# Performance work log

Measured on AMD Instinct MI355X. Metric: run time of the kernel, lower is better.

## Reference

```python
import jax, jax.numpy as jnp
import numpy as np

N = 100000        # number of nodes
D_IN = 256        # input feature dim
D_OUT = 128       # output feature dim
NNZ_X = 3200000   # features_nonzero
NNZ_A = 3200000   # adjacency nnz (avg degree 32)
DROPOUT = 0.1


def setup_inputs() -> dict:
    key = jax.random.key(0)
    ks = jax.random.split(key, 7)
    x_rows = jax.random.randint(ks[0], (NNZ_X,), 0, N, dtype=jnp.int32)
    x_cols = jax.random.randint(ks[1], (NNZ_X,), 0, D_IN, dtype=jnp.int32)
    x_vals = jax.random.normal(ks[2], (NNZ_X,), dtype=jnp.float32)
    adj_rows = jax.random.randint(ks[3], (NNZ_A,), 0, N, dtype=jnp.int32)
    adj_cols = jax.random.randint(ks[4], (NNZ_A,), 0, N, dtype=jnp.int32)
    adj_vals = jax.random.uniform(ks[5], (NNZ_A,), dtype=jnp.float32)  # normalized-adj-like positive weights
    W = jax.random.normal(ks[6], (D_IN, D_OUT), dtype=jnp.float32) * 0.05  # 'random_normal' init
    return {"x_rows": x_rows, "x_cols": x_cols, "x_vals": x_vals,
            "adj_rows": adj_rows, "adj_cols": adj_cols, "adj_vals": adj_vals,
            "W": W}


def reference(x_rows, x_cols, x_vals, adj_rows, adj_cols, adj_vals, W):
    keep_prob = 1.0 - DROPOUT
    # tf: dropout_mask = floor(keep_prob + uniform) -> Bernoulli(keep_prob) in {0,1}
    mask = jnp.floor(keep_prob + jax.random.uniform(jax.random.key(42), x_vals.shape, dtype=x_vals.dtype))
    xv = x_vals * mask * (1.0 / keep_prob)  # sparse dropout: retain + rescale
    # SpMM 1: x @ W  -> h [N, D_OUT]; gather W rows by column index, scatter-add by row index
    h = jax.ops.segment_sum(xv[:, None] * W[x_cols], x_rows, num_segments=N)
    # SpMM 2: adj @ h -> out [N, D_OUT]
    out = jax.ops.segment_sum(adj_vals[:, None] * h[adj_cols], adj_rows, num_segments=N)
    return jax.nn.relu(out)
```

## Files before the change

kernel.cpp:

```cpp
#include <hip/hip_runtime.h>
#include <hip/hip_fp16.h>
#include <stdint.h>

constexpr int kN    = 100000;
constexpr int kDOut = 128;
constexpr int kDIn  = 256;
constexpr int kNNZ  = 3200000;
constexpr float kInvKeep = (float)(1.0 / 0.9);
constexpr int kCopies = 8;

typedef __attribute__((ext_vector_type(8))) short short8v;
typedef __attribute__((ext_vector_type(4))) float f32x4;

__device__ __forceinline__ uint32_t rotl32(uint32_t v, int r) {
  return (v << r) | (v >> (32 - r));
}
__device__ __forceinline__ void threefry2x32(uint32_t k0, uint32_t k1,
                                             uint32_t x0, uint32_t x1,
                                             uint32_t& o0, uint32_t& o1) {
  const uint32_t ks0 = k0, ks1 = k1, ks2 = k0 ^ k1 ^ 0x1BD11BDAu;
  x0 += ks0; x1 += ks1;
#define TF_RND(r) { x0 += x1; x1 = rotl32(x1, (r)); x1 ^= x0; }
  TF_RND(13) TF_RND(15) TF_RND(26) TF_RND(6)
  x0 += ks1; x1 += ks2 + 1u;
  TF_RND(17) TF_RND(29) TF_RND(16) TF_RND(24)
  x0 += ks2; x1 += ks0 + 2u;
  TF_RND(13) TF_RND(15) TF_RND(26) TF_RND(6)
  x0 += ks0; x1 += ks1 + 3u;
  TF_RND(17) TF_RND(29) TF_RND(16) TF_RND(24)
  x0 += ks1; x1 += ks2 + 4u;
  TF_RND(13) TF_RND(15) TF_RND(26) TF_RND(6)
  x0 += ks2; x1 += ks0 + 5u;
#undef TF_RND
  o0 = x0; o1 = x1;
}
__device__ __forceinline__ float keep_mask(uint32_t i) {
  uint32_t o0, o1;
  threefry2x32(0u, 42u, 0u, i, o0, o1);
  uint32_t bits = o0 ^ o1;
  float u = __uint_as_float((bits >> 9) | 0x3f800000u) - 1.0f;
  return floorf(0.9f + u);
}

__device__ __forceinline__ uint32_t f32_to_bf16(float f) {
  uint32_t u = __float_as_uint(f);
  u += 0x7fffu + ((u >> 16) & 1u);
  return u >> 16;
}
__device__ __forceinline__ float bf16lo_to_f32(uint32_t packed) {
  return __uint_as_float(packed << 16);
}
__device__ __forceinline__ float bf16hi_to_f32(uint32_t packed) {
  return __uint_as_float(packed & 0xffff0000u);
}

__global__ void wpack_frag_kernel(const float* __restrict__ W,
                                  uint32_t* __restrict__ Wt) {
  int i = blockIdx.x * blockDim.x + threadIdx.x;
  if (i >= kDIn * kDOut / 2) return;
  int jj   = i & 3;
  int lane = (i >> 2) & 63;
  int ks   = (i >> 8) & 7;
  int nt   = i >> 11;
  int n = nt * 16 + (lane & 15);
  int k = ks * 32 + ((lane >> 4) * 8) + 2 * jj;
  uint32_t lo = f32_to_bf16(W[(size_t)k * kDOut + n]);
  uint32_t hi = f32_to_bf16(W[(size_t)(k + 1) * kDOut + n]);
  Wt[i] = lo | (hi << 16);
}

__global__ void scatteradd_kernel(const int* __restrict__ rows,
                                  const int* __restrict__ cols,
                                  const float* __restrict__ vals,
                                  float* __restrict__ Xd, int nnz) {
  int e = blockIdx.x * blockDim.x + threadIdx.x;
  if (e >= nnz) return;
  if (keep_mask((uint32_t)e) == 0.0f) return;
  atomicAdd(&Xd[(size_t)rows[e] * kDIn + cols[e]], vals[e] * kInvKeep);
}

__global__ void __launch_bounds__(256) gemm_mfma_kernel(
    const float* __restrict__ Xd, const uint32_t* __restrict__ Wt,
    uint16_t* __restrict__ hb) {
  const int tid = threadIdx.x;
  const int gw = blockIdx.x * 4 + (tid >> 6);
  if (gw >= kN / 16) return;
  const int lane = tid & 63;
  const int row16 = gw * 16;
  const float* xrow = Xd + (size_t)(row16 + (lane & 15)) * kDIn + ((lane >> 4) * 8);

  f32x4 acc[8];
  #pragma unroll
  for (int nt = 0; nt < 8; ++nt) acc[nt] = f32x4{0.f, 0.f, 0.f, 0.f};

  #pragma unroll
  for (int ks = 0; ks < 8; ++ks) {
    float4 xa = *(const float4*)(xrow + ks * 32);
    float4 xb = *(const float4*)(xrow + ks * 32 + 4);
    short8v a;
    a[0] = (short)f32_to_bf16(xa.x); a[1] = (short)f32_to_bf16(xa.y);
    a[2] = (short)f32_to_bf16(xa.z); a[3] = (short)f32_to_bf16(xa.w);
    a[4] = (short)f32_to_bf16(xb.x); a[5] = (short)f32_to_bf16(xb.y);
    a[6] = (short)f32_to_bf16(xb.z); a[7] = (short)f32_to_bf16(xb.w);
    const uint32_t* bbase = Wt + ks * 256 + lane * 4;
    #pragma unroll
    for (int nt = 0; nt < 8; ++nt) {
      short8v b = *(const short8v*)(bbase + nt * 2048);
      acc[nt] = __builtin_amdgcn_mfma_f32_16x16x32_bf16(a, b, acc[nt], 0, 0, 0);
    }
  }

  const int r0 = row16 + (lane >> 4) * 4;
  const int c0 = lane & 15;
  #pragma unroll
  for (int nt = 0; nt < 8; ++nt) {
    #pragma unroll
    for (int rg = 0; rg < 4; ++rg) {
      hb[(size_t)(r0 + rg) * kDOut + nt * 16 + c0] =
          (uint16_t)f32_to_bf16(acc[nt][rg]);
    }
  }
}

__global__ void hist8_kernel(const int* __restrict__ rows, int* __restrict__ cnt8,
                             int nnz) {
  int e = blockIdx.x * blockDim.x + threadIdx.x;
  if (e >= nnz) return;
  int k = blockIdx.x & (kCopies - 1);
  atomicAdd(&cnt8[k * kN + rows[e]], 1);
}

constexpr int kScanChunk = 2048;
constexpr int kScanBlk   = (kN + kScanChunk - 1) / kScanChunk;

__global__ void scan1_kernel(const int* __restrict__ cnt8, int* __restrict__ rowptr,
                             int* __restrict__ partials, int n) {
  __shared__ int sd[256];
  int b = blockIdx.x, t = threadIdx.x;
  int base = b * kScanChunk + t * 8;
  int v[8]; int s = 0;
  #pragma unroll
  for (int k = 0; k < 8; ++k) {
    int idx = base + k;
    int c = 0;
    if (idx < n) {
      #pragma unroll
      for (int j = 0; j < kCopies; ++j) c += cnt8[j * kN + idx];
    }
    v[k] = c; s += c;
  }
  sd[t] = s; __syncthreads();
  #pragma unroll
  for (int off = 1; off < 256; off <<= 1) {
    int x = (t >= off) ? sd[t - off] : 0;
    __syncthreads();
    sd[t] += x;
    __syncthreads();
  }
  if (t == 255) partials[b] = sd[255];
  int run = (t == 0) ? 0 : sd[t - 1];
  #pragma unroll
  for (int k = 0; k < 8; ++k) { int idx = base + k; if (idx < n) rowptr[idx] = run; run += v[k]; }
}

__global__ void scan2_kernel(int* __restrict__ partials, int* __restrict__ rowptr,
                             int nblk, int n) {
  __shared__ int sd[64];
  int t = threadIdx.x;
  sd[t] = (t < nblk) ? partials[t] : 0;
  __syncthreads();
  #pragma unroll
  for (int off = 1; off < 64; off <<= 1) {
    int x = (t >= off) ? sd[t - off] : 0;
    __syncthreads();
    sd[t] += x;
    __syncthreads();
  }
  if (t < nblk) partials[t] = (t == 0) ? 0 : sd[t - 1];
  if (t == 63) rowptr[n] = sd[63];
}

__global__ void scan3_kernel(int* __restrict__ rowptr, int* __restrict__ cur,
                             const int* __restrict__ partials, int n) {
  int i = blockIdx.x * blockDim.x + threadIdx.x;
  if (i < n) {
    int v = rowptr[i] + partials[i / kScanChunk];
    rowptr[i] = v;
    cur[i] = v;
  }
}

__global__ void scatter_adj_kernel(const int* __restrict__ rows,
                                   const int* __restrict__ cols,
                                   const float* __restrict__ vals,
                                   int* __restrict__ cur,
                                   uint32_t* __restrict__ spack, int nnz) {
  int e = blockIdx.x * blockDim.x + threadIdx.x;
  if (e >= nnz) return;
  float v = vals[e];
  int pos = atomicAdd(&cur[rows[e]], 1);
  uint32_t h = (uint32_t)__half_as_ushort(__float2half_rn(v)) & 0x7FFFu;
  spack[pos] = ((uint32_t)cols[e] << 15) | h;
}

template<bool RELU>
__global__ void spmm_csr_kernel(const int* __restrict__ rowptr,
                                const uint32_t* __restrict__ spack,
                                const uint16_t* __restrict__ B,
                                float* __restrict__ outv, int nrows) {
  int tid = threadIdx.x;
  int row = blockIdx.x * 4 + (tid >> 6);
  int lane = tid & 63;
  if (row >= nrows) return;
  int e = rowptr[row], e_end = rowptr[row + 1];
  float a0 = 0.0f, a1 = 0.0f;
  const int doff = lane * 2;
  auto dec = [](uint32_t p) -> float {
    return __half2float(__ushort_as_half((unsigned short)(p & 0x7FFFu)));
  };
  for (; e + 7 < e_end; e += 8) {
    uint32_t p0 = spack[e],     p1 = spack[e + 1];
    uint32_t p2 = spack[e + 2], p3 = spack[e + 3];
    uint32_t p4 = spack[e + 4], p5 = spack[e + 5];
    uint32_t p6 = spack[e + 6], p7 = spack[e + 7];
    uint32_t g0 = *(const uint32_t*)(B + (size_t)(p0 >> 15) * kDOut + doff);
    uint32_t g1 = *(const uint32_t*)(B + (size_t)(p1 >> 15) * kDOut + doff);
    uint32_t g2 = *(const uint32_t*)(B + (size_t)(p2 >> 15) * kDOut + doff);
    uint32_t g3 = *(const uint32_t*)(B + (size_t)(p3 >> 15) * kDOut + doff);
    uint32_t g4 = *(const uint32_t*)(B + (size_t)(p4 >> 15) * kDOut + doff);
    uint32_t g5 = *(const uint32_t*)(B + (size_t)(p5 >> 15) * kDOut + doff);
    uint32_t g6 = *(const uint32_t*)(B + (size_t)(p6 >> 15) * kDOut + doff);
    uint32_t g7 = *(const uint32_t*)(B + (size_t)(p7 >> 15) * kDOut + doff);
    float v0 = dec(p0), v1 = dec(p1), v2 = dec(p2), v3 = dec(p3);
    float v4 = dec(p4), v5 = dec(p5), v6 = dec(p6), v7 = dec(p7);
    a0 += v0 * bf16lo_to_f32(g0); a1 += v0 * bf16hi_to_f32(g0);
    a0 += v1 * bf16lo_to_f32(g1); a1 += v1 * bf16hi_to_f32(g1);
    a0 += v2 * bf16lo_to_f32(g2); a1 += v2 * bf16hi_to_f32(g2);
    a0 += v3 * bf16lo_to_f32(g3); a1 += v3 * bf16hi_to_f32(g3);
    a0 += v4 * bf16lo_to_f32(g4); a1 += v4 * bf16hi_to_f32(g4);
    a0 += v5 * bf16lo_to_f32(g5); a1 += v5 * bf16hi_to_f32(g5);
    a0 += v6 * bf16lo_to_f32(g6); a1 += v6 * bf16hi_to_f32(g6);
    a0 += v7 * bf16lo_to_f32(g7); a1 += v7 * bf16hi_to_f32(g7);
  }
  for (; e < e_end; ++e) {
    uint32_t p0 = spack[e];
    float v0 = dec(p0);
    uint32_t g0 = *(const uint32_t*)(B + (size_t)(p0 >> 15) * kDOut + doff);
    a0 += v0 * bf16lo_to_f32(g0);
    a1 += v0 * bf16hi_to_f32(g0);
  }
  if (RELU) { a0 = fmaxf(a0, 0.0f); a1 = fmaxf(a1, 0.0f); }
  float2 o; o.x = a0; o.y = a1;
  ((float2*)outv)[(size_t)row * (kDOut / 2) + lane] = o;
}

extern "C" void kernel_launch(void* const* d_in, const int* in_sizes, int n_in,
                              void* d_out, int out_size, void* d_ws, size_t ws_size,
                              hipStream_t stream) {
  const int*   x_rows   = (const int*)d_in[0];
  const int*   x_cols   = (const int*)d_in[1];
  const float* x_vals   = (const float*)d_in[2];
  const int*   adj_rows = (const int*)d_in[3];
  const int*   adj_cols = (const int*)d_in[4];
  const float* adj_vals = (const float*)d_in[5];
  const float* W        = (const float*)d_in[6];
  float* out = (float*)d_out;

  size_t off = 0;
  auto take = [&](size_t bytes) -> char* {
    char* p = (char*)d_ws + off;
    off += (bytes + 255) & ~(size_t)255;
    return p;
  };
  uint16_t* hb     = (uint16_t*)take((size_t)kN * kDOut * 2);
  uint32_t* Wt     = (uint32_t*)take((size_t)kDIn * kDOut / 2 * 4);
  int*      rowptr = (int*)take((size_t)(kN + 1) * 4);
  int*      cnt8   = (int*)take((size_t)kCopies * kN * 4);
  int*      cur    = (int*)take((size_t)kN * 4);
  int*      partials = (int*)take(64 * 4);
  uint32_t* spack  = (uint32_t*)take((size_t)kNNZ * 4);
  float*    Xd     = (float*)take((size_t)kN * kDIn * 4);
  const size_t needed = off;
  if (ws_size < needed) return;

  const int edgeBlocks = (kNNZ + 255) / 256;
  const int spmmBlocks = (kN + 3) / 4;
  const int gemmBlocks = (kN / 16 + 3) / 4;

  wpack_frag_kernel<<<(kDIn * kDOut / 2 + 255) / 256, 256, 0, stream>>>(W, Wt);

  hipMemsetAsync(Xd, 0, (size_t)kN * kDIn * 4, stream);
  scatteradd_kernel<<<edgeBlocks, 256, 0, stream>>>(x_rows, x_cols, x_vals, Xd, kNNZ);
  gemm_mfma_kernel<<<gemmBlocks, 256, 0, stream>>>(Xd, Wt, hb);

  hipMemsetAsync(cnt8, 0, (size_t)kCopies * kN * 4, stream);
  hist8_kernel<<<edgeBlocks, 256, 0, stream>>>(adj_rows, cnt8, kNNZ);
  scan1_kernel<<<kScanBlk, 256, 0, stream>>>(cnt8, rowptr, partials, kN);
  scan2_kernel<<<1, 64, 0, stream>>>(partials, rowptr, kScanBlk, kN);
  scan3_kernel<<<(kN + 255) / 256, 256, 0, stream>>>(rowptr, cur, partials, kN);
  scatter_adj_kernel<<<edgeBlocks, 256, 0, stream>>>(
      adj_rows, adj_cols, adj_vals, cur, spack, kNNZ);
  spmm_csr_kernel<true><<<spmmBlocks, 256, 0, stream>>>(
      rowptr, spack, hb, out, kN);
}
```

Measured before the change: 668.9 us.

## Split adjacency CSR scatter into two-pass bucketed partition for locality

```diff
diff --git a/kernel.cpp b/kernel.cpp
--- a/kernel.cpp
+++ b/kernel.cpp
@@ -7,7 +7,8 @@
 constexpr int kDIn  = 256;
 constexpr int kNNZ  = 3200000;
 constexpr float kInvKeep = (float)(1.0 / 0.9);
-constexpr int kCopies = 8;
+constexpr int kCopies  = 8;
+constexpr int kBktRows = kN / 8;
 
 typedef __attribute__((ext_vector_type(8))) short short8v;
 typedef __attribute__((ext_vector_type(4))) float f32x4;
@@ -181,26 +182,86 @@
 }
 
 __global__ void scan3_kernel(int* __restrict__ rowptr, int* __restrict__ cur,
+                             int* __restrict__ bcur,
                              const int* __restrict__ partials, int n) {
   int i = blockIdx.x * blockDim.x + threadIdx.x;
   if (i < n) {
     int v = rowptr[i] + partials[i / kScanChunk];
     rowptr[i] = v;
     cur[i] = v;
-  }
-}
-
-__global__ void scatter_adj_kernel(const int* __restrict__ rows,
-                                   const int* __restrict__ cols,
-                                   const float* __restrict__ vals,
-                                   int* __restrict__ cur,
-                                   uint32_t* __restrict__ spack, int nnz) {
-  int e = blockIdx.x * blockDim.x + threadIdx.x;
-  if (e >= nnz) return;
-  float v = vals[e];
-  int pos = atomicAdd(&cur[rows[e]], 1);
-  uint32_t h = (uint32_t)__half_as_ushort(__float2half_rn(v)) & 0x7FFFu;
-  spack[pos] = ((uint32_t)cols[e] << 15) | h;
+    if ((i % kBktRows) == 0) bcur[i / kBktRows] = v;
+  }
+}
+
+__global__ void __launch_bounds__(256) passA_kernel(
+    const int* __restrict__ rows, const int* __restrict__ cols,
+    const float* __restrict__ vals, int* __restrict__ bcur,
+    uint2* __restrict__ P, int nnz) {
+  __shared__ int lcnt[8];
+  __shared__ int gbase[8];
+  const int tid = threadIdx.x;
+  const int base = blockIdx.x * 4096;
+  if (tid < 8) lcnt[tid] = 0;
+  __syncthreads();
+  int c0 = 0, c1 = 0, c2 = 0, c3 = 0, c4 = 0, c5 = 0, c6 = 0, c7 = 0;
+  for (int i = 0; i < 16; ++i) {
+    int e = base + i * 256 + tid;
+    if (e < nnz) {
+      int b = rows[e] / kBktRows;
+      if (b < 4) {
+        if (b < 2) { if (b == 0) c0++; else c1++; }
+        else       { if (b == 2) c2++; else c3++; }
+      } else {
+        if (b < 6) { if (b == 4) c4++; else c5++; }
+        else       { if (b == 6) c6++; else c7++; }
+      }
+    }
+  }
+  if (c0) atomicAdd(&lcnt[0], c0);
+  if (c1) atomicAdd(&lcnt[1], c1);
+  if (c2) atomicAdd(&lcnt[2], c2);
+  if (c3) atomicAdd(&lcnt[3], c3);
+  if (c4) atomicAdd(&lcnt[4], c4);
+  if (c5) atomicAdd(&lcnt[5], c5);
+  if (c6) atomicAdd(&lcnt[6], c6);
+  if (c7) atomicAdd(&lcnt[7], c7);
+  __syncthreads();
+  if (tid < 8) {
+    gbase[tid] = atomicAdd(&bcur[tid], lcnt[tid]);
+    lcnt[tid] = 0;
+  }
+  __syncthreads();
+  for (int i = 0; i < 16; ++i) {
+    int e = base + i * 256 + tid;
+    if (e >= nnz) continue;
+    int r = rows[e];
+    int b = r / kBktRows;
+    int lpos = atomicAdd(&lcnt[b], 1);
+    uint2 rec;
+    rec.x = ((uint32_t)(r % kBktRows) << 17) | (uint32_t)cols[e];
+    rec.y = __float_as_uint(vals[e]);
+    P[gbase[b] + lpos] = rec;
+  }
+}
+
+__global__ void passB_kernel(const int* __restrict__ rowptr,
+                             const uint2* __restrict__ P,
+                             int* __restrict__ cur,
+                             uint32_t* __restrict__ spack) {
+  const int k = blockIdx.x & 7;
+  const int slot = blockIdx.x >> 3;
+  const int nslots = gridDim.x >> 3;
+  const int lorow = k * kBktRows;
+  const int s = rowptr[lorow];
+  const int t = rowptr[lorow + kBktRows];
+  for (int idx = s + slot * 256 + threadIdx.x; idx < t; idx += nslots * 256) {
+    uint2 rec = P[idx];
+    int r = lorow + (int)(rec.x >> 17);
+    int pos = atomicAdd(&cur[r], 1);
+    float v = __uint_as_float(rec.y);
+    uint32_t h = (uint32_t)__half_as_ushort(__float2half_rn(v)) & 0x7FFFu;
+    spack[pos] = ((rec.x & 0x1FFFFu) << 15) | h;
+  }
 }
 
 template<bool RELU>
@@ -277,15 +338,19 @@
   int*      rowptr = (int*)take((size_t)(kN + 1) * 4);
   int*      cnt8   = (int*)take((size_t)kCopies * kN * 4);
   int*      cur    = (int*)take((size_t)kN * 4);
+  int*      bcur   = (int*)take(8 * 4);
   int*      partials = (int*)take(64 * 4);
   uint32_t* spack  = (uint32_t*)take((size_t)kNNZ * 4);
   float*    Xd     = (float*)take((size_t)kN * kDIn * 4);
   const size_t needed = off;
   if (ws_size < needed) return;
+  uint2*    P = (uint2*)Xd;
 
   const int edgeBlocks = (kNNZ + 255) / 256;
   const int spmmBlocks = (kN + 3) / 4;
   const int gemmBlocks = (kN / 16 + 3) / 4;
+  const int passABlocks = (kNNZ + 4095) / 4096;
+  const int passBBlocks = 8 * 1664;
 
   wpack_frag_kernel<<<(kDIn * kDOut / 2 + 255) / 256, 256, 0, stream>>>(W, Wt);
 
@@ -297,9 +362,10 @@
   hist8_kernel<<<edgeBlocks, 256, 0, stream>>>(adj_rows, cnt8, kNNZ);
   scan1_kernel<<<kScanBlk, 256, 0, stream>>>(cnt8, rowptr, partials, kN);
   scan2_kernel<<<1, 64, 0, stream>>>(partials, rowptr, kScanBlk, kN);
-  scan3_kernel<<<(kN + 255) / 256, 256, 0, stream>>>(rowptr, cur, partials, kN);
-  scatter_adj_kernel<<<edgeBlocks, 256, 0, stream>>>(
-      adj_rows, adj_cols, adj_vals, cur, spack, kNNZ);
+  scan3_kernel<<<(kN + 255) / 256, 256, 0, stream>>>(rowptr, cur, bcur, partials, kN);
+  passA_kernel<<<passABlocks, 256, 0, stream>>>(
+      adj_rows, adj_cols, adj_vals, bcur, P, kNNZ);
+  passB_kernel<<<passBBlocks, 256, 0, stream>>>(rowptr, P, cur, spack);
   spmm_csr_kernel<true><<<spmmBlocks, 256, 0, stream>>>(
       rowptr, spack, hb, out, kN);
 }
```

After: 625.3 us. 6.5% less time.
